# Kernel tuning notes

Hardware: AMD Instinct MI355X
Metric: run time of the kernel (lower is better)

Reference implementation:

```python
import jax, jax.numpy as jnp
import numpy as np

D_MODEL = 128
NUM_CLASSES = 32
ETA = 4.0
RC = 6.0
NR = 4          # ceil(D_MODEL / NUM_CLASSES)
# lmax = floor(sqrt(NR-1)) = 1 -> spherical harmonics l=0 and l=1 (4 components)


def setup_inputs() -> dict:
    key = jax.random.key(0)
    k1, k2 = jax.random.split(key)
    B, N = 256, 1024
    xyz = jax.random.normal(k1, (B, N, 3), dtype=jnp.float32) * 2.0
    cls = jax.random.randint(k2, (B, N), 0, NUM_CLASSES).astype(jnp.float32)
    x = jnp.concatenate([xyz, cls[..., None]], axis=-1)  # [B,N,4]
    return {"x": x}


def _forward(x):
    Rs = jnp.arange(NR, dtype=x.dtype) * (RC / NR)       # [NR] = [0,1.5,3,4.5]
    xyz = x[..., :3]
    r = jnp.sqrt(jnp.sum(xyz * xyz, axis=-1))            # [B,N]

    # radial basis: exp(-eta*(Rs - r)^2)                  -> [B,N,NR]
    radial = jnp.exp(-ETA * (Rs - r[..., None]) ** 2)

    # cosine cutoff (r clamped to Rc -> weight 0 beyond)  -> [B,N,1]
    rc = jnp.minimum(r, RC)
    env = (0.5 * jnp.cos(jnp.pi * rc / RC) + 0.5)[..., None]

    # real spherical harmonics l<=1 on unit directions, orthonormal norm,
    # m ordering (-l..l): [Y00, Y1,-1~y, Y1,0~z, Y1,1~x]  -> [B,N,NR]
    u = xyz / jnp.where(r > 0, r, 1.0)[..., None]
    y00 = 0.5 / jnp.sqrt(jnp.pi)
    c1 = jnp.sqrt(3.0 / (4.0 * jnp.pi))
    sh = jnp.stack(
        [jnp.full(r.shape, y00, dtype=x.dtype),
         c1 * u[..., 1], c1 * u[..., 2], c1 * u[..., 0]], axis=-1)

    prod = sh * radial * env                             # [B,N,NR]

    # per-class masked scatter: pos[b,n,:,c] = prod[b,n,:] where class==c and r!=0
    cls = x[..., 3].astype(jnp.int32)
    onehot = jax.nn.one_hot(cls, NUM_CLASSES, dtype=prod.dtype) * (r != 0)[..., None]
    pos = prod[..., :, None] * onehot[..., None, :]      # [B,N,NR,C]
    B, N = x.shape[0], x.shape[1]
    pos = pos.reshape(B, N, NR * NUM_CLASSES)[..., :D_MODEL]

    pos = jnp.nan_to_num(pos, nan=0.0)

    # torch F.normalize default dim=1 (neighbor axis), eps=1e-12
    norm = jnp.sqrt(jnp.sum(pos * pos, axis=1, keepdims=True))
    pos = pos / jnp.maximum(norm, 1e-12)

    # standardize along feature axis (torch std is unbiased, ddof=1)
    mean = jnp.mean(pos, axis=-1, keepdims=True)
    std = jnp.std(pos, axis=-1, ddof=1, keepdims=True)
    return (pos - mean) / (std + 1e-6)


def reference(x):
    return _forward(x)
```

## Files before the change

### kernel.cpp

```cpp
#include <hip/hip_runtime.h>
#include <math.h>

#define B_SZ 256
#define N_SZ 1024
#define D_MODEL 128
#define NUM_CLASSES 32

#define K_EXP (-5.770780163555854f)
#define K_COS (1.0f / 12.0f)

__device__ __forceinline__ void compute_prod(const float4 xv, float& r, int& c, float p[4]) {
    const float y00 = 0.28209479177387814f;
    const float c1  = 0.48860251190291992f;
    float r2 = xv.x * xv.x + xv.y * xv.y + xv.z * xv.z;
    r = sqrtf(r2);
    c = (int)xv.w;
    float inv_r = (r > 0.0f) ? __builtin_amdgcn_rcpf(r) : 0.0f;
    float ux = xv.x * inv_r, uy = xv.y * inv_r, uz = xv.z * inv_r;
    float rc = fminf(r, 6.0f);
    float env = 0.5f * __builtin_amdgcn_cosf(rc * K_COS) + 0.5f;
    float d0 = 0.0f - r, d1 = 1.5f - r, d2 = 3.0f - r, d3 = 4.5f - r;
    float rad0 = __builtin_amdgcn_exp2f(d0 * d0 * K_EXP);
    float rad1 = __builtin_amdgcn_exp2f(d1 * d1 * K_EXP);
    float rad2 = __builtin_amdgcn_exp2f(d2 * d2 * K_EXP);
    float rad3 = __builtin_amdgcn_exp2f(d3 * d3 * K_EXP);
    p[0] = y00 * rad0 * env;
    p[1] = c1 * uy * rad1 * env;
    p[2] = c1 * uz * rad2 * env;
    p[3] = c1 * ux * rad3 * env;
}

__global__ __launch_bounds__(1024) void ape_fused_kernel(const float* __restrict__ x,
                                                         float* __restrict__ out) {
    __shared__ float nsq[D_MODEL];
    __shared__ float invn[D_MODEL];
    __shared__ float sp0[N_SZ], sp1[N_SZ], sp2[N_SZ], sp3[N_SZ];
    __shared__ int   scls[N_SZ];
    __shared__ float4 samb[N_SZ];
    __shared__ float2 sbc[N_SZ];

    const int b = blockIdx.x;
    const int t = threadIdx.x;
    if (t < D_MODEL) nsq[t] = 0.0f;
    __syncthreads();

    {
        float4 xv = ((const float4*)x)[(size_t)b * N_SZ + t];
        float r; int c; float p[4];
        compute_prod(xv, r, c, p);
        if (r <= 0.0f) { p[0] = p[1] = p[2] = p[3] = 0.0f; }
        sp0[t] = p[0]; sp1[t] = p[1]; sp2[t] = p[2]; sp3[t] = p[3];
        scls[t] = c;
        if (r > 0.0f) {
            atomicAdd(&nsq[0 * NUM_CLASSES + c], p[0] * p[0]);
            atomicAdd(&nsq[1 * NUM_CLASSES + c], p[1] * p[1]);
            atomicAdd(&nsq[2 * NUM_CLASSES + c], p[2] * p[2]);
            atomicAdd(&nsq[3 * NUM_CLASSES + c], p[3] * p[3]);
        }
    }
    __syncthreads();

    if (t < D_MODEL) {
        invn[t] = __builtin_amdgcn_rcpf(fmaxf(sqrtf(nsq[t]), 1e-12f));
    }
    __syncthreads();

    {
        const int c = scls[t];
        float pn0 = sp0[t] * invn[0 * NUM_CLASSES + c];
        float pn1 = sp1[t] * invn[1 * NUM_CLASSES + c];
        float pn2 = sp2[t] * invn[2 * NUM_CLASSES + c];
        float pn3 = sp3[t] * invn[3 * NUM_CLASSES + c];
        float sum = pn0 + pn1 + pn2 + pn3;
        float mean = sum * (1.0f / 128.0f);
        float sumsq = pn0 * pn0 + pn1 * pn1 + pn2 * pn2 + pn3 * pn3;
        float var = fmaxf((sumsq - 128.0f * mean * mean) * (1.0f / 127.0f), 0.0f);
        float inv_std = __builtin_amdgcn_rcpf(sqrtf(var) + 1e-6f);
        float bneg = -mean * inv_std;
        samb[t] = make_float4(pn0 * inv_std + bneg,
                              pn1 * inv_std + bneg,
                              pn2 * inv_std + bneg,
                              pn3 * inv_std + bneg);
        sbc[t] = make_float2(bneg, __int_as_float(c));
    }
    __syncthreads();

    {
        const int lane = t & 31;
        const int grp  = t >> 5;
        const int qsel = lane >> 3;
        const int m    = (lane & 7) * 4;
        const float* samb_f = (const float*)samb;
        float4* op = (float4*)out + ((size_t)b * N_SZ + grp) * 32 + lane;
#pragma unroll
        for (int k = 0; k < 32; ++k) {
            const int n = (k << 5) + grp;
            const float a  = samb_f[(n << 2) + qsel];
            const float2 bc = sbc[n];
            const float bneg = bc.x;
            const int   c    = __float_as_int(bc.y);
            float4 o;
            o.x = (c == m + 0) ? a : bneg;
            o.y = (c == m + 1) ? a : bneg;
            o.z = (c == m + 2) ? a : bneg;
            o.w = (c == m + 3) ? a : bneg;
            op[k * (32 * 32)] = o;
        }
    }
}

extern "C" void kernel_launch(void* const* d_in, const int* in_sizes, int n_in,
                              void* d_out, int out_size, void* d_ws, size_t ws_size,
                              hipStream_t stream) {
    const float* x = (const float*)d_in[0];
    float* out = (float*)d_out;
    ape_fused_kernel<<<B_SZ, 1024, 0, stream>>>(x, out);
}
```

Before: 140.6 us.

## Split fused kernel into norm pass and wider-grid store pass

Splits the single per-batch kernel into two launches: one computes per-class inverse norms into workspace, and a second with four times as many smaller blocks recomputes the features and writes the output. The aim is more parallelism and better occupancy for the write-dominated store phase, since the old version had only 256 large blocks. In exchange it reads the input twice, recomputes the transcendental features, and pays for an extra launch.

```diff
diff --git a/kernel.cpp b/kernel.cpp
--- a/kernel.cpp
+++ b/kernel.cpp
@@ -5,6 +5,7 @@
 #define N_SZ 1024
 #define D_MODEL 128
 #define NUM_CLASSES 32
+#define PPB 256
 
 #define K_EXP (-5.770780163555854f)
 #define K_COS (1.0f / 12.0f)
@@ -30,47 +31,55 @@
     p[3] = c1 * ux * rad3 * env;
 }
 
-__global__ __launch_bounds__(1024) void ape_fused_kernel(const float* __restrict__ x,
-                                                         float* __restrict__ out) {
+__global__ __launch_bounds__(1024) void ape_norm_kernel(const float* __restrict__ x,
+                                                        float* __restrict__ invn_g) {
     __shared__ float nsq[D_MODEL];
-    __shared__ float invn[D_MODEL];
-    __shared__ float sp0[N_SZ], sp1[N_SZ], sp2[N_SZ], sp3[N_SZ];
-    __shared__ int   scls[N_SZ];
-    __shared__ float4 samb[N_SZ];
-    __shared__ float2 sbc[N_SZ];
-
     const int b = blockIdx.x;
     const int t = threadIdx.x;
     if (t < D_MODEL) nsq[t] = 0.0f;
     __syncthreads();
 
-    {
-        float4 xv = ((const float4*)x)[(size_t)b * N_SZ + t];
-        float r; int c; float p[4];
-        compute_prod(xv, r, c, p);
-        if (r <= 0.0f) { p[0] = p[1] = p[2] = p[3] = 0.0f; }
-        sp0[t] = p[0]; sp1[t] = p[1]; sp2[t] = p[2]; sp3[t] = p[3];
-        scls[t] = c;
-        if (r > 0.0f) {
-            atomicAdd(&nsq[0 * NUM_CLASSES + c], p[0] * p[0]);
-            atomicAdd(&nsq[1 * NUM_CLASSES + c], p[1] * p[1]);
-            atomicAdd(&nsq[2 * NUM_CLASSES + c], p[2] * p[2]);
-            atomicAdd(&nsq[3 * NUM_CLASSES + c], p[3] * p[3]);
-        }
+    float4 xv = ((const float4*)x)[(size_t)b * N_SZ + t];
+    float r; int c; float p[4];
+    compute_prod(xv, r, c, p);
+    if (r > 0.0f) {
+        atomicAdd(&nsq[0 * NUM_CLASSES + c], p[0] * p[0]);
+        atomicAdd(&nsq[1 * NUM_CLASSES + c], p[1] * p[1]);
+        atomicAdd(&nsq[2 * NUM_CLASSES + c], p[2] * p[2]);
+        atomicAdd(&nsq[3 * NUM_CLASSES + c], p[3] * p[3]);
     }
     __syncthreads();
 
     if (t < D_MODEL) {
-        invn[t] = __builtin_amdgcn_rcpf(fmaxf(sqrtf(nsq[t]), 1e-12f));
+        invn_g[(size_t)b * D_MODEL + t] =
+            __builtin_amdgcn_rcpf(fmaxf(sqrtf(nsq[t]), 1e-12f));
     }
+}
+
+__global__ __launch_bounds__(256) void ape_store_kernel(const float* __restrict__ x,
+                                                        const float* __restrict__ invn_g,
+                                                        float* __restrict__ out) {
+    __shared__ float invn[D_MODEL];
+    __shared__ float4 samb[PPB];
+    __shared__ float2 sbc[PPB];
+
+    const int b  = blockIdx.x >> 2;
+    const int n0 = (blockIdx.x & 3) << 8;
+    const int t  = threadIdx.x;
+
+    if (t < D_MODEL) invn[t] = invn_g[(size_t)b * D_MODEL + t];
     __syncthreads();
 
     {
-        const int c = scls[t];
-        float pn0 = sp0[t] * invn[0 * NUM_CLASSES + c];
-        float pn1 = sp1[t] * invn[1 * NUM_CLASSES + c];
-        float pn2 = sp2[t] * invn[2 * NUM_CLASSES + c];
-        float pn3 = sp3[t] * invn[3 * NUM_CLASSES + c];
+        const int n = n0 + t;
+        float4 xv = ((const float4*)x)[(size_t)b * N_SZ + n];
+        float r; int c; float p[4];
+        compute_prod(xv, r, c, p);
+        if (r <= 0.0f) { p[0] = p[1] = p[2] = p[3] = 0.0f; }
+        float pn0 = p[0] * invn[0 * NUM_CLASSES + c];
+        float pn1 = p[1] * invn[1 * NUM_CLASSES + c];
+        float pn2 = p[2] * invn[2 * NUM_CLASSES + c];
+        float pn3 = p[3] * invn[3 * NUM_CLASSES + c];
         float sum = pn0 + pn1 + pn2 + pn3;
         float mean = sum * (1.0f / 128.0f);
         float sumsq = pn0 * pn0 + pn1 * pn1 + pn2 * pn2 + pn3 * pn3;
@@ -91,11 +100,11 @@
         const int qsel = lane >> 3;
         const int m    = (lane & 7) * 4;
         const float* samb_f = (const float*)samb;
-        float4* op = (float4*)out + ((size_t)b * N_SZ + grp) * 32 + lane;
+        float4* op = (float4*)out + ((size_t)b * N_SZ + n0 + grp) * 32 + lane;
 #pragma unroll
-        for (int k = 0; k < 32; ++k) {
-            const int n = (k << 5) + grp;
-            const float a  = samb_f[(n << 2) + qsel];
+        for (int k = 0; k < PPB / 8; ++k) {
+            const int n = (k << 3) + grp;
+            const float a   = samb_f[(n << 2) + qsel];
             const float2 bc = sbc[n];
             const float bneg = bc.x;
             const int   c    = __float_as_int(bc.y);
@@ -104,7 +113,7 @@
             o.y = (c == m + 1) ? a : bneg;
             o.z = (c == m + 2) ? a : bneg;
             o.w = (c == m + 3) ? a : bneg;
-            op[k * (32 * 32)] = o;
+            op[(size_t)k * (8 * 32)] = o;
         }
     }
 }
@@ -114,5 +123,7 @@
                               hipStream_t stream) {
     const float* x = (const float*)d_in[0];
     float* out = (float*)d_out;
-    ape_fused_kernel<<<B_SZ, 1024, 0, stream>>>(x, out);
+    float* invn_g = (float*)d_ws;
+    ape_norm_kernel<<<B_SZ, 1024, 0, stream>>>(x, invn_g);
+    ape_store_kernel<<<B_SZ * (N_SZ / PPB), 256, 0, stream>>>(x, invn_g, out);
 }
```

After: 140.7 us. No clear change (+0.1%).
